# Kernel tuning notes

Hardware: AMD Instinct MI355X
Metric: run time of the kernel (lower is better)

The kernel has to match this reference:

```python
import jax, jax.numpy as jnp
import numpy as np

B, N, D = 2, 2048, 768
H = 12
HD = D // H
SCALE = HD ** -0.5
EPS = 1e-8


def exp0(v, c):
    # Poincare exponential map at origin: tanh(sqrt(c)||v||) * v / (sqrt(c)||v||)
    sc = jnp.sqrt(c)
    n = jnp.sqrt(jnp.sum(v * v, axis=-1, keepdims=True))
    n = jnp.maximum(n, EPS)
    return jnp.tanh(sc * n) * v / (sc * n)


def log0(x, c):
    # Poincare log map at origin: artanh(sqrt(c)||x||) * x / (sqrt(c)||x||)
    sc = jnp.sqrt(c)
    n = jnp.sqrt(jnp.sum(x * x, axis=-1, keepdims=True))
    n = jnp.maximum(n, EPS)
    t = jnp.clip(sc * n, 0.0, 1.0 - 1e-7)
    return jnp.arctanh(t) * x / (sc * n)


def setup_inputs() -> dict:
    key = jax.random.key(0)
    k1, k2, k3 = jax.random.split(key, 3)
    c0 = 0.1
    x = jax.random.normal(k1, (B, N, D), dtype=jnp.float32)
    # rescale so sqrt(c)*||x|| = 0.5 -> valid points strictly inside the ball
    xn = jnp.sqrt(jnp.sum(x * x, axis=-1, keepdims=True))
    x = x * (0.5 / (np.sqrt(c0) * jnp.maximum(xn, EPS)))
    w_qkv = jax.random.normal(k2, (3 * D, D), dtype=jnp.float32) * (D ** -0.5)
    w_proj = jax.random.normal(k3, (D, D), dtype=jnp.float32) * (D ** -0.5)
    b_proj = jnp.zeros((D,), dtype=jnp.float32)
    curvature = jnp.asarray(c0, dtype=jnp.float32)
    return {"x": x, "w_qkv": w_qkv, "w_proj": w_proj, "b_proj": b_proj,
            "curvature": curvature}


def reference(x, w_qkv, w_proj, b_proj, curvature):
    c = curvature
    v = log0(x, c)                                   # [B,N,D] tangent vectors
    qkv = jnp.einsum('bnd,ed->bne', v, w_qkv)        # [B,N,3D]
    qkv = qkv.reshape(B, N, 3, H, HD).transpose(2, 0, 3, 1, 4)  # [3,B,H,N,HD]
    q, k, v_proj = qkv[0], qkv[1], qkv[2]
    # Map q,k back onto the manifold for the hyperbolic distance score
    qm = exp0(q, c)                                  # [B,H,N,HD]
    km = exp0(k, c)
    q_nsq = jnp.sum(qm * qm, axis=-1)                # [B,H,N]
    k_nsq = jnp.sum(km * km, axis=-1)                # [B,H,N]
    dot = jnp.einsum('bhnd,bhmd->bhnm', qm, km)      # [B,H,N,N]
    # ||q-k||^2 = ||q||^2 + ||k||^2 - 2 q.k  (avoids [B,H,N,N,HD] intermediate)
    diff_sq = jnp.maximum(q_nsq[..., :, None] + k_nsq[..., None, :] - 2.0 * dot, 0.0)
    q_cl = jnp.minimum(q_nsq, 0.99)
    k_cl = jnp.minimum(k_nsq, 0.99)
    denom = (1.0 - q_cl)[..., :, None] * (1.0 - k_cl)[..., None, :] + 1e-8
    inner = jnp.maximum(1.0 + 2.0 * diff_sq / denom, 1.0 + 1e-7)
    distances = jnp.arccosh(inner)                   # [B,H,N,N]
    scores = -distances * SCALE
    attn = jax.nn.softmax(scores, axis=-1)
    out = jnp.einsum('bhnm,bhmd->bhnd', attn, v_proj)
    out = out.transpose(0, 2, 1, 3).reshape(B, N, D)
    v_out = jnp.einsum('bnd,ed->bne', out, w_proj) + b_proj
    return exp0(v_out, c)                            # [B,N,D] on manifold
```

## Files before the change

kernel.cpp:

```cpp
#include <hip/hip_runtime.h>
#include <cmath>

#define ROWS 4096
#define DIM 768
#define QKV_COLS 2304
#define NHEAD 12
#define HEAD_DIM 64
#define SEQ 2048

static constexpr float EPS_F = 1e-8f;

typedef __bf16 bfrag __attribute__((ext_vector_type(8)));
typedef float  f32x4 __attribute__((ext_vector_type(4)));

__device__ __forceinline__ float wave_sum64(float v) {
#pragma unroll
  for (int off = 1; off < 64; off <<= 1) v += __shfl_xor(v, off, 64);
  return v;
}

__device__ __forceinline__ unsigned short f2bf(float f) {
  unsigned u = __float_as_uint(f);
  u += 0x7fffu + ((u >> 16) & 1u);
  return (unsigned short)(u >> 16);
}

__device__ __forceinline__ float tanh_over_x(float x) {
  const float e  = __builtin_amdgcn_exp2f(x * 2.8853900817779268f);
  const float th = (e - 1.0f) * __builtin_amdgcn_rcpf(e + 1.0f);
  return (x < 1e-4f) ? 1.0f : th * __builtin_amdgcn_rcpf(x);
}

__device__ __forceinline__ void gl_lds16(const void* g, void* l) {
  __builtin_amdgcn_global_load_lds((const __attribute__((address_space(1))) void*)g,
                                   (__attribute__((address_space(3))) void*)l, 16, 0, 0);
}

__global__ __launch_bounds__(256) void log0_conv(const float* __restrict__ x,
                                                 const float* __restrict__ cptr,
                                                 unsigned short* __restrict__ vout,
                                                 const float* __restrict__ wa, int na,
                                                 const float* __restrict__ wb, int nb,
                                                 unsigned short* __restrict__ da,
                                                 unsigned short* __restrict__ db) {
  if (blockIdx.x >= ROWS / 4) {
    const int i = ((blockIdx.x - ROWS / 4) * 256 + threadIdx.x) * 4;
    const float* s;
    unsigned short* d;
    int j;
    if (i < na) { s = wa; d = da; j = i; }
    else { j = i - na; if (j >= nb) return; s = wb; d = db; }
    const float4 v = *(const float4*)(s + j);
    ushort4 o;
    o.x = f2bf(v.x); o.y = f2bf(v.y); o.z = f2bf(v.z); o.w = f2bf(v.w);
    *(ushort4*)(d + j) = o;
    return;
  }
  const int lane = threadIdx.x & 63;
  const int row  = (blockIdx.x << 2) + (threadIdx.x >> 6);
  const float* xr = x + (size_t)row * DIM;
  unsigned short* vr = vout + (size_t)row * DIM;
  float vals[12];
  float ss = 0.f;
#pragma unroll
  for (int i = 0; i < 12; ++i) {
    float t = xr[lane + (i << 6)];
    vals[i] = t;
    ss += t * t;
  }
  ss = wave_sum64(ss);
  const float sc  = sqrtf(cptr[0]);
  const float n   = fmaxf(sqrtf(ss), EPS_F);
  const float scn = sc * n;
  const float t   = fminf(scn, 1.0f - 1e-7f);
  const float ath = 0.34657359027997264f *
                    __builtin_amdgcn_logf((1.0f + t) * __builtin_amdgcn_rcpf(1.0f - t));
  const float f   = (scn < 1e-4f) ? 1.0f : ath * __builtin_amdgcn_rcpf(scn);
#pragma unroll
  for (int i = 0; i < 12; ++i) vr[lane + (i << 6)] = f2bf(vals[i] * f);
}

__global__ __launch_bounds__(256) void exp0_out_kernel(const float* __restrict__ vin,
                                                       const float* __restrict__ cptr,
                                                       float* __restrict__ outp) {
  const int lane = threadIdx.x & 63;
  const int row  = (blockIdx.x << 2) + (threadIdx.x >> 6);
  const float* vr = vin + (size_t)row * DIM;
  float* orow = outp + (size_t)row * DIM;
  float vals[12];
  float ss = 0.f;
#pragma unroll
  for (int i = 0; i < 12; ++i) {
    float t = vr[lane + (i << 6)];
    vals[i] = t;
    ss += t * t;
  }
  ss = wave_sum64(ss);
  const float sc = sqrtf(cptr[0]);
  const float n  = fmaxf(sqrtf(ss), EPS_F);
  const float f  = tanh_over_x(sc * n);
#pragma unroll
  for (int i = 0; i < 12; ++i) orow[lane + (i << 6)] = vals[i] * f;
}

template<int BM, int BN>
__global__ __launch_bounds__(256) void gemm_nt_dbuf(const unsigned short* __restrict__ A,
                                                    const unsigned short* __restrict__ B,
                                                    float* __restrict__ C,
                                                    int M, int Ncols, int K,
                                                    const float* __restrict__ bias) {
  constexpr int FI = BM / 32;
  constexpr int FJ = BN / 32;
  constexpr int CH = BM / 64;
  __shared__ unsigned short As[2][BM * 32];
  __shared__ unsigned short Bs[2][BN * 32];
  const int tid = threadIdx.x;
  const int w = tid >> 6, lane = tid & 63;
  const int lq = lane & 15, quad = lane >> 4;
  const int wr = w >> 1, wc = w & 1;
  const int row0 = blockIdx.y * BM;
  const int col0 = blockIdx.x * BN;
  const int srow  = lane >> 2;
  const int skoff = (lane & 3) << 3;

  f32x4 acc[FI][FJ];
#pragma unroll
  for (int i = 0; i < FI; ++i)
#pragma unroll
    for (int j = 0; j < FJ; ++j) acc[i][j] = (f32x4){0.f, 0.f, 0.f, 0.f};

  auto pf = [&](int k0, int buf) {
#pragma unroll
    for (int c = 0; c < CH; ++c) {
      const int r = c * 64 + w * 16;
      gl_lds16(A + (size_t)(row0 + r + srow) * K + k0 + skoff, &As[buf][r * 32]);
      gl_lds16(B + (size_t)(col0 + r + srow) * K + k0 + skoff, &Bs[buf][r * 32]);
    }
  };

  pf(0, 0);
  const int NIT = K / 32;
  for (int it = 0; it < NIT; ++it) {
    const int buf = it & 1;
    __syncthreads();
    if (it + 1 < NIT) pf((it + 1) * 32, buf ^ 1);

    bfrag af[FI], bfg[FJ];
#pragma unroll
    for (int i = 0; i < FI; ++i)
      af[i] = *(const bfrag*)&As[buf][(wr * (BM / 2) + i * 16 + lq) * 32 + (quad << 3)];
#pragma unroll
    for (int j = 0; j < FJ; ++j)
      bfg[j] = *(const bfrag*)&Bs[buf][(wc * (BN / 2) + j * 16 + lq) * 32 + (quad << 3)];
#pragma unroll
    for (int i = 0; i < FI; ++i)
#pragma unroll
      for (int j = 0; j < FJ; ++j)
        acc[i][j] = __builtin_amdgcn_mfma_f32_16x16x32_bf16(af[i], bfg[j], acc[i][j], 0, 0, 0);
  }

#pragma unroll
  for (int i = 0; i < FI; ++i) {
    const int crow = row0 + wr * (BM / 2) + i * 16 + (quad << 2);
#pragma unroll
    for (int j = 0; j < FJ; ++j) {
      const int col = col0 + wc * (BN / 2) + j * 16 + lq;
      const float bj = bias ? bias[col] : 0.0f;
      float* cp = C + (size_t)crow * Ncols + col;
#pragma unroll
      for (int r = 0; r < 4; ++r)
        cp[(size_t)r * Ncols] = acc[i][j][r] + bj;
    }
  }
}

__global__ __launch_bounds__(256) void gemm_qkv_fused(const unsigned short* __restrict__ A,
                                                      const unsigned short* __restrict__ B,
                                                      const float* __restrict__ cptr,
                                                      unsigned short* __restrict__ qh,
                                                      unsigned short* __restrict__ kh,
                                                      unsigned short* __restrict__ vth,
                                                      float* __restrict__ qnA,
                                                      float* __restrict__ qnB,
                                                      float* __restrict__ knA,
                                                      float* __restrict__ knB) {
  __shared__ unsigned short As[2][128 * 32];
  __shared__ unsigned short Bs[2][128 * 32];
  const int tid = threadIdx.x;
  const int w = tid >> 6, lane = tid & 63;
  const int lq = lane & 15, quad = lane >> 4;
  const int wr = w >> 1, wc = w & 1;
  const int row0 = blockIdx.y << 7;
  const int col0 = blockIdx.x << 7;
  const int srow  = lane >> 2;
  const int skoff = (lane & 3) << 3;

  f32x4 acc[4][4];
#pragma unroll
  for (int i = 0; i < 4; ++i)
#pragma unroll
    for (int j = 0; j < 4; ++j) acc[i][j] = (f32x4){0.f, 0.f, 0.f, 0.f};

  auto pf = [&](int k0, int buf) {
#pragma unroll
    for (int c = 0; c < 2; ++c) {
      const int r = c * 64 + w * 16;
      gl_lds16(A + (size_t)(row0 + r + srow) * DIM + k0 + skoff, &As[buf][r * 32]);
      gl_lds16(B + (size_t)(col0 + r + srow) * DIM + k0 + skoff, &Bs[buf][r * 32]);
    }
  };

  pf(0, 0);
  for (int it = 0; it < DIM / 32; ++it) {
    const int buf = it & 1;
    __syncthreads();
    if (it + 1 < DIM / 32) pf((it + 1) * 32, buf ^ 1);

    bfrag af[4], bfg[4];
#pragma unroll
    for (int i = 0; i < 4; ++i)
      af[i] = *(const bfrag*)&As[buf][((wr << 6) + (i << 4) + lq) * 32 + (quad << 3)];
#pragma unroll
    for (int j = 0; j < 4; ++j)
      bfg[j] = *(const bfrag*)&Bs[buf][((wc << 6) + (j << 4) + lq) * 32 + (quad << 3)];
#pragma unroll
    for (int i = 0; i < 4; ++i)
#pragma unroll
      for (int j = 0; j < 4; ++j)
        acc[i][j] = __builtin_amdgcn_mfma_f32_16x16x32_bf16(af[i], bfg[j], acc[i][j], 0, 0, 0);
  }

  const int colw = col0 + (wc << 6);
  const int seg  = colw / DIM;
  const int hh   = (colw % DIM) >> 6;
  const int rowb = row0 + (wr << 6);

  if (seg == 2) {
#pragma unroll
    for (int i = 0; i < 4; ++i)
#pragma unroll
      for (int r = 0; r < 4; ++r) {
        const int rowg = rowb + (i << 4) + (quad << 2) + r;
        const int bh = (rowg >> 11) * NHEAD + hh;
        const int n_ = rowg & 2047;
#pragma unroll
        for (int j = 0; j < 4; ++j)
          vth[((size_t)bh * HEAD_DIM + (j << 4) + lq) * SEQ + n_] = f2bf(acc[i][j][r]);
      }
  } else {
    unsigned short* dst = seg ? kh : qh;
    float* nA = seg ? knA : qnA;
    float* nB = seg ? knB : qnB;
    const float sc = sqrtf(cptr[0]);
#pragma unroll
    for (int i = 0; i < 4; ++i)
#pragma unroll
      for (int r = 0; r < 4; ++r) {
        float ss = acc[i][0][r] * acc[i][0][r];
        ss = fmaf(acc[i][1][r], acc[i][1][r], ss);
        ss = fmaf(acc[i][2][r], acc[i][2][r], ss);
        ss = fmaf(acc[i][3][r], acc[i][3][r], ss);
        ss += __shfl_xor(ss, 1, 64);
        ss += __shfl_xor(ss, 2, 64);
        ss += __shfl_xor(ss, 4, 64);
        ss += __shfl_xor(ss, 8, 64);
        const float nn = fmaxf(sqrtf(ss), EPS_F);
        const float f  = tanh_over_x(sc * nn);
        const int rowg = rowb + (i << 4) + (quad << 2) + r;
        const int bh = (rowg >> 11) * NHEAD + hh;
        const int n_ = rowg & 2047;
        unsigned short* rp = dst + ((size_t)bh * SEQ + n_) * HEAD_DIM;
#pragma unroll
        for (int j = 0; j < 4; ++j)
          rp[(j << 4) + lq] = f2bf(acc[i][j][r] * f);
        if (lq == 0) {
          const float nrm = ss * f * f;
          nA[(size_t)bh * SEQ + n_] = nrm;
          nB[(size_t)bh * SEQ + n_] = 1.0f / (1.0f - fminf(nrm, 0.99f));
        }
      }
  }
}

__global__ __launch_bounds__(256) void flash_mfma(const unsigned short* __restrict__ qh,
                                                  const unsigned short* __restrict__ kh,
                                                  const unsigned short* __restrict__ vth,
                                                  const float* __restrict__ qnA,
                                                  const float* __restrict__ qnB,
                                                  const float* __restrict__ knA,
                                                  const float* __restrict__ knB,
                                                  unsigned short* __restrict__ attn_out) {
  const int flat = blockIdx.x;
  const int bhid = flat % 24;
  const int qt   = flat / 24;
  const int h = bhid % NHEAD, b = bhid / NHEAD;
  const int bh = b * NHEAD + h;
  const int tid = threadIdx.x;
  const int w = tid >> 6, lane = tid & 63;
  const int lq = lane & 15, quad = lane >> 4;

  __shared__ unsigned short Ks[2][64 * 64];
  __shared__ unsigned short Vt[2][64 * 64];
  __shared__ unsigned short Ps[64 * 64];

  const unsigned short* qbase = qh + ((size_t)bh * SEQ + (size_t)qt * 64) * HEAD_DIM;
  const float* knAb = knA + (size_t)bh * SEQ;
  const float* knBb = knB + (size_t)bh * SEQ;

  const int srow = tid >> 3, spos = tid & 7;
  const int sB = spos ^ (srow & 7);
  const char* kgsrc = (const char*)(kh + (size_t)bh * SEQ * HEAD_DIM) + (size_t)srow * 128 + sB * 16;
  const char* vgsrc = (const char*)(vth + (size_t)bh * HEAD_DIM * SEQ) + (size_t)srow * 4096 + sB * 16;

  auto prefetch = [&](int kt, int buf) {
    const char* kp = kgsrc + (size_t)kt * 8192;
    const char* vp = vgsrc + (size_t)kt * 128;
    gl_lds16(kp,          (char*)Ks[buf] + w * 1024);
    gl_lds16(kp + 4096,   (char*)Ks[buf] + 4096 + w * 1024);
    gl_lds16(vp,          (char*)Vt[buf] + w * 1024);
    gl_lds16(vp + 131072, (char*)Vt[buf] + 4096 + w * 1024);
  };

  bfrag aq[2];
#pragma unroll
  for (int khf = 0; khf < 2; ++khf)
    aq[khf] = *(const bfrag*)(qbase + (size_t)(w * 16 + lq) * HEAD_DIM + khf * 32 + quad * 8);

  const float qnS = qnA[(size_t)bh * SEQ + qt * 64 + w * 16 + lq];
  const float rqS = 2.0f * qnB[(size_t)bh * SEQ + qt * 64 + w * 16 + lq];

  bfrag ones;
#pragma unroll
  for (int j = 0; j < 8; ++j) ones[j] = (__bf16)1.0f;

  f32x4 oacc[4];
  f32x4 lacc = (f32x4){0.f, 0.f, 0.f, 0.f};
#pragma unroll
  for (int d = 0; d < 4; ++d) oacc[d] = (f32x4){0.f, 0.f, 0.f, 0.f};
  const int swz = lq & 7;

  prefetch(0, 0);
  for (int kt = 0; kt < SEQ / 64; ++kt) {
    const int buf = kt & 1;
    const int key0 = kt * 64;
    __syncthreads();
    if (kt + 1 < SEQ / 64) prefetch(kt + 1, buf ^ 1);

    f32x4 kna[4], knr[4];
#pragma unroll
    for (int st = 0; st < 4; ++st) {
      kna[st] = *(const f32x4*)(knAb + key0 + st * 16 + (quad << 2));
      knr[st] = *(const f32x4*)(knBb + key0 + st * 16 + (quad << 2));
    }

    f32x4 s[4];
#pragma unroll
    for (int st = 0; st < 4; ++st) s[st] = (f32x4){0.f, 0.f, 0.f, 0.f};
#pragma unroll
    for (int khf = 0; khf < 2; ++khf)
#pragma unroll
      for (int st = 0; st < 4; ++st) {
        const bfrag ak = *(const bfrag*)&Ks[buf][(st * 16 + lq) * 64 + (((khf << 2) + quad) ^ swz) * 8];
        s[st] = __builtin_amdgcn_mfma_f32_16x16x32_bf16(ak, aq[khf], s[st], 0, 0, 0);
      }

#pragma unroll
    for (int st = 0; st < 4; ++st) {
      unsigned u[4];
#pragma unroll
      for (int i = 0; i < 4; ++i) {
        float tt = fmaf(-2.0f, s[st][i], qnS + kna[st][i]);
        tt = fmaxf(tt, 0.0f);
        const float inner = fmaf(tt, rqS * knr[st][i], 1.0f);
        const float root = __builtin_amdgcn_sqrtf(fmaf(inner, inner, -1.0f));
        const float wgt = __builtin_amdgcn_exp2f(-0.125f * __builtin_amdgcn_logf(inner + root));
        u[i] = __float_as_uint(wgt);
      }
      uint2 pk;
      pk.x = __builtin_amdgcn_perm(u[1], u[0], 0x07060302u);
      pk.y = __builtin_amdgcn_perm(u[3], u[2], 0x07060302u);
      *(uint2*)&Ps[(((w * 16 + lq) << 6) + st * 16 + quad * 4) ^ (swz << 3)] = pk;
    }

#pragma unroll
    for (int khf = 0; khf < 2; ++khf) {
      const bfrag ap = *(const bfrag*)&Ps[(((w * 16 + lq) << 6) + khf * 32 + quad * 8) ^ (swz << 3)];
      lacc = __builtin_amdgcn_mfma_f32_16x16x32_bf16(ap, ones, lacc, 0, 0, 0);
#pragma unroll
      for (int d = 0; d < 4; ++d) {
        const bfrag bv = *(const bfrag*)&Vt[buf][(d * 16 + lq) * 64 + (((khf << 2) + quad) ^ swz) * 8];
        oacc[d] = __builtin_amdgcn_mfma_f32_16x16x32_bf16(ap, bv, oacc[d], 0, 0, 0);
      }
    }
  }

  float rl4[4];
#pragma unroll
  for (int i = 0; i < 4; ++i) rl4[i] = __builtin_amdgcn_rcpf(lacc[i]);

  unsigned short* ob = attn_out + ((size_t)b * SEQ + (size_t)qt * 64 + w * 16) * DIM + h * HEAD_DIM;
#pragma unroll
  for (int d = 0; d < 4; ++d)
#pragma unroll
    for (int i = 0; i < 4; ++i)
      ob[(size_t)(quad * 4 + i) * DIM + d * 16 + lq] = f2bf(oacc[d][i] * rl4[i]);
}

extern "C" void kernel_launch(void* const* d_in, const int* in_sizes, int n_in,
                              void* d_out, int out_size, void* d_ws, size_t ws_size,
                              hipStream_t stream) {
  const float* x      = (const float*)d_in[0];
  const float* w_qkv  = (const float*)d_in[1];
  const float* w_proj = (const float*)d_in[2];
  const float* b_proj = (const float*)d_in[3];
  const float* curv   = (const float*)d_in[4];
  float* outp = (float*)d_out;

  float* ws = (float*)d_ws;
  unsigned short* v_tan_bf = (unsigned short*)ws;
  unsigned short* attn_bf  = (unsigned short*)ws;
  float* v_out = ws + 1572864;
  unsigned short* qh  = (unsigned short*)(v_out + 3145728);
  unsigned short* kh  = qh + 3145728;
  unsigned short* vth = kh + 3145728;
  unsigned short* wqkv_bf  = vth + 3145728;
  unsigned short* wproj_bf = wqkv_bf + 1769472;
  float* qnA = (float*)(wproj_bf + 589824);
  float* qnB = qnA + 49152;
  float* knA = qnB + 49152;
  float* knB = knA + 49152;

  log0_conv<<<dim3(ROWS / 4 + 2304), dim3(256), 0, stream>>>(
      x, curv, v_tan_bf, w_qkv, 1769472, w_proj, 589824, wqkv_bf, wproj_bf);
  gemm_qkv_fused<<<dim3(QKV_COLS / 128, ROWS / 128), dim3(256), 0, stream>>>(
      v_tan_bf, wqkv_bf, curv, qh, kh, vth, qnA, qnB, knA, knB);
  flash_mfma<<<dim3(768), dim3(256), 0, stream>>>(qh, kh, vth, qnA, qnB, knA, knB, attn_bf);
  gemm_nt_dbuf<64, 64><<<dim3(DIM / 64, ROWS / 64), dim3(256), 0, stream>>>(
      attn_bf, wproj_bf, v_out, ROWS, DIM, DIM, b_proj);
  exp0_out_kernel<<<dim3(ROWS / 4), dim3(256), 0, stream>>>(v_out, curv, outp);
}
```

Baseline: 205.2 us.

## Split attention key range across two wave groups per block and merge partials

New measurement: 197.1 us. -3.9%, faster.

```diff
diff --git a/kernel.cpp b/kernel.cpp
--- a/kernel.cpp
+++ b/kernel.cpp
@@ -282,14 +282,14 @@
   }
 }
 
-__global__ __launch_bounds__(256) void flash_mfma(const unsigned short* __restrict__ qh,
-                                                  const unsigned short* __restrict__ kh,
-                                                  const unsigned short* __restrict__ vth,
-                                                  const float* __restrict__ qnA,
-                                                  const float* __restrict__ qnB,
-                                                  const float* __restrict__ knA,
-                                                  const float* __restrict__ knB,
-                                                  unsigned short* __restrict__ attn_out) {
+__global__ __launch_bounds__(512, 6) void flash_mfma(const unsigned short* __restrict__ qh,
+                                                     const unsigned short* __restrict__ kh,
+                                                     const unsigned short* __restrict__ vth,
+                                                     const float* __restrict__ qnA,
+                                                     const float* __restrict__ qnB,
+                                                     const float* __restrict__ knA,
+                                                     const float* __restrict__ knB,
+                                                     unsigned short* __restrict__ attn_out) {
   const int flat = blockIdx.x;
   const int bhid = flat % 24;
   const int qt   = flat / 24;
@@ -298,36 +298,40 @@
   const int tid = threadIdx.x;
   const int w = tid >> 6, lane = tid & 63;
   const int lq = lane & 15, quad = lane >> 4;
-
-  __shared__ unsigned short Ks[2][64 * 64];
-  __shared__ unsigned short Vt[2][64 * 64];
-  __shared__ unsigned short Ps[64 * 64];
+  const int wq = w & 3;
+  const int wh = w >> 2;
+
+  __shared__ __align__(16) unsigned short Ks[2][2][32 * 64];
+  __shared__ __align__(16) unsigned short Vt[2][2][64 * 32];
+  __shared__ __align__(16) unsigned short Ps[8][16 * 32];
 
   const unsigned short* qbase = qh + ((size_t)bh * SEQ + (size_t)qt * 64) * HEAD_DIM;
   const float* knAb = knA + (size_t)bh * SEQ;
   const float* knBb = knB + (size_t)bh * SEQ;
-
-  const int srow = tid >> 3, spos = tid & 7;
-  const int sB = spos ^ (srow & 7);
-  const char* kgsrc = (const char*)(kh + (size_t)bh * SEQ * HEAD_DIM) + (size_t)srow * 128 + sB * 16;
-  const char* vgsrc = (const char*)(vth + (size_t)bh * HEAD_DIM * SEQ) + (size_t)srow * 4096 + sB * 16;
+  const char* khb = (const char*)(kh + (size_t)bh * SEQ * HEAD_DIM);
+  const char* vtb = (const char*)(vth + (size_t)bh * HEAD_DIM * SEQ);
+
+  const int krow = lane >> 3;
+  const int koff = ((wq << 3) + krow) * 128 + (((lane & 7) ^ krow) << 4);
+  const int c     = (wq << 6) + lane;
+  const int vrow2 = c >> 3;
+  const int vd    = (vrow2 << 1) + ((c >> 2) & 1);
+  const int vg    = (c & 3) ^ (vrow2 & 3);
+  const size_t voffb = (size_t)vd * (SEQ * 2);
 
   auto prefetch = [&](int kt, int buf) {
-    const char* kp = kgsrc + (size_t)kt * 8192;
-    const char* vp = vgsrc + (size_t)kt * 128;
-    gl_lds16(kp,          (char*)Ks[buf] + w * 1024);
-    gl_lds16(kp + 4096,   (char*)Ks[buf] + 4096 + w * 1024);
-    gl_lds16(vp,          (char*)Vt[buf] + w * 1024);
-    gl_lds16(vp + 131072, (char*)Vt[buf] + 4096 + w * 1024);
+    const int kb = (wh << 10) + (kt << 5);
+    gl_lds16(khb + (size_t)kb * 128 + koff, (char*)&Ks[wh][buf][0] + (wq << 10));
+    gl_lds16(vtb + voffb + (size_t)(kb + (vg << 3)) * 2, (char*)&Vt[wh][buf][0] + (wq << 10));
   };
 
   bfrag aq[2];
 #pragma unroll
   for (int khf = 0; khf < 2; ++khf)
-    aq[khf] = *(const bfrag*)(qbase + (size_t)(w * 16 + lq) * HEAD_DIM + khf * 32 + quad * 8);
-
-  const float qnS = qnA[(size_t)bh * SEQ + qt * 64 + w * 16 + lq];
-  const float rqS = 2.0f * qnB[(size_t)bh * SEQ + qt * 64 + w * 16 + lq];
+    aq[khf] = *(const bfrag*)(qbase + (size_t)((wq << 4) + lq) * HEAD_DIM + khf * 32 + quad * 8);
+
+  const float qnS = qnA[(size_t)bh * SEQ + qt * 64 + (wq << 4) + lq];
+  const float rqS = 2.0f * qnB[(size_t)bh * SEQ + qt * 64 + (wq << 4) + lq];
 
   bfrag ones;
 #pragma unroll
@@ -338,34 +342,36 @@
 #pragma unroll
   for (int d = 0; d < 4; ++d) oacc[d] = (f32x4){0.f, 0.f, 0.f, 0.f};
   const int swz = lq & 7;
+  const int vsw = (lq >> 1) & 3;
+  const int psx = ((lq >> 2) & 3) << 3;
 
   prefetch(0, 0);
-  for (int kt = 0; kt < SEQ / 64; ++kt) {
+  for (int kt = 0; kt < 32; ++kt) {
     const int buf = kt & 1;
-    const int key0 = kt * 64;
+    const int key0 = (wh << 10) + (kt << 5);
     __syncthreads();
-    if (kt + 1 < SEQ / 64) prefetch(kt + 1, buf ^ 1);
-
-    f32x4 kna[4], knr[4];
-#pragma unroll
-    for (int st = 0; st < 4; ++st) {
+    if (kt + 1 < 32) prefetch(kt + 1, buf ^ 1);
+
+    f32x4 kna[2], knr[2];
+#pragma unroll
+    for (int st = 0; st < 2; ++st) {
       kna[st] = *(const f32x4*)(knAb + key0 + st * 16 + (quad << 2));
       knr[st] = *(const f32x4*)(knBb + key0 + st * 16 + (quad << 2));
     }
 
-    f32x4 s[4];
-#pragma unroll
-    for (int st = 0; st < 4; ++st) s[st] = (f32x4){0.f, 0.f, 0.f, 0.f};
+    f32x4 s[2];
+#pragma unroll
+    for (int st = 0; st < 2; ++st) s[st] = (f32x4){0.f, 0.f, 0.f, 0.f};
 #pragma unroll
     for (int khf = 0; khf < 2; ++khf)
 #pragma unroll
-      for (int st = 0; st < 4; ++st) {
-        const bfrag ak = *(const bfrag*)&Ks[buf][(st * 16 + lq) * 64 + (((khf << 2) + quad) ^ swz) * 8];
+      for (int st = 0; st < 2; ++st) {
+        const bfrag ak = *(const bfrag*)&Ks[wh][buf][(st * 16 + lq) * 64 + (((khf << 2) + quad) ^ swz) * 8];
         s[st] = __builtin_amdgcn_mfma_f32_16x16x32_bf16(ak, aq[khf], s[st], 0, 0, 0);
       }
 
 #pragma unroll
-    for (int st = 0; st < 4; ++st) {
+    for (int st = 0; st < 2; ++st) {
       unsigned u[4];
 #pragma unroll
       for (int i = 0; i < 4; ++i) {
@@ -379,26 +385,44 @@
       uint2 pk;
       pk.x = __builtin_amdgcn_perm(u[1], u[0], 0x07060302u);
       pk.y = __builtin_amdgcn_perm(u[3], u[2], 0x07060302u);
-      *(uint2*)&Ps[(((w * 16 + lq) << 6) + st * 16 + quad * 4) ^ (swz << 3)] = pk;
-    }
-
-#pragma unroll
-    for (int khf = 0; khf < 2; ++khf) {
-      const bfrag ap = *(const bfrag*)&Ps[(((w * 16 + lq) << 6) + khf * 32 + quad * 8) ^ (swz << 3)];
-      lacc = __builtin_amdgcn_mfma_f32_16x16x32_bf16(ap, ones, lacc, 0, 0, 0);
-#pragma unroll
-      for (int d = 0; d < 4; ++d) {
-        const bfrag bv = *(const bfrag*)&Vt[buf][(d * 16 + lq) * 64 + (((khf << 2) + quad) ^ swz) * 8];
-        oacc[d] = __builtin_amdgcn_mfma_f32_16x16x32_bf16(ap, bv, oacc[d], 0, 0, 0);
-      }
-    }
+      *(uint2*)&Ps[w][(lq << 5) + (((st << 4) + (quad << 2)) ^ psx)] = pk;
+    }
+
+    const bfrag ap = *(const bfrag*)&Ps[w][(lq << 5) + ((quad << 3) ^ psx)];
+    lacc = __builtin_amdgcn_mfma_f32_16x16x32_bf16(ap, ones, lacc, 0, 0, 0);
+#pragma unroll
+    for (int d = 0; d < 4; ++d) {
+      const int dd = (d << 4) + lq;
+      const bfrag bv = *(const bfrag*)&Vt[wh][buf][(dd >> 1) * 64 + (dd & 1) * 32 + (quad ^ vsw) * 8];
+      oacc[d] = __builtin_amdgcn_mfma_f32_16x16x32_bf16(ap, bv, oacc[d], 0, 0, 0);
+    }
+  }
+
+  __syncthreads();
+  float* cb = (float*)&Ks[0][0][0];
+  float* lb = (float*)&Vt[0][0][0];
+  const int ci = (wq << 6) + lane;
+  if (wh) {
+    float* p = cb + ci * 16;
+#pragma unroll
+    for (int d = 0; d < 4; ++d) *(f32x4*)(p + (d << 2)) = oacc[d];
+    *(f32x4*)(lb + (ci << 2)) = lacc;
+  }
+  __syncthreads();
+  if (wh) return;
+
+  {
+    const float* p = cb + ci * 16;
+#pragma unroll
+    for (int d = 0; d < 4; ++d) oacc[d] += *(const f32x4*)(p + (d << 2));
+    lacc += *(const f32x4*)(lb + (ci << 2));
   }
 
   float rl4[4];
 #pragma unroll
   for (int i = 0; i < 4; ++i) rl4[i] = __builtin_amdgcn_rcpf(lacc[i]);
 
-  unsigned short* ob = attn_out + ((size_t)b * SEQ + (size_t)qt * 64 + w * 16) * DIM + h * HEAD_DIM;
+  unsigned short* ob = attn_out + ((size_t)b * SEQ + (size_t)qt * 64 + (wq << 4)) * DIM + h * HEAD_DIM;
 #pragma unroll
   for (int d = 0; d < 4; ++d)
 #pragma unroll
@@ -434,7 +458,7 @@
       x, curv, v_tan_bf, w_qkv, 1769472, w_proj, 589824, wqkv_bf, wproj_bf);
   gemm_qkv_fused<<<dim3(QKV_COLS / 128, ROWS / 128), dim3(256), 0, stream>>>(
       v_tan_bf, wqkv_bf, curv, qh, kh, vth, qnA, qnB, knA, knB);
-  flash_mfma<<<dim3(768), dim3(256), 0, stream>>>(qh, kh, vth, qnA, qnB, knA, knB, attn_bf);
+  flash_mfma<<<dim3(768), dim3(512), 0, stream>>>(qh, kh, vth, qnA, qnB, knA, knB, attn_bf);
   gemm_nt_dbuf<64, 64><<<dim3(DIM / 64, ROWS / 64), dim3(256), 0, stream>>>(
       attn_bf, wproj_bf, v_out, ROWS, DIM, DIM, b_proj);
   exp0_out_kernel<<<dim3(ROWS / 4), dim3(256), 0, stream>>>(v_out, curv, outp);
```
